# Kernel tuning notes

Hardware: AMD Instinct MI355X
Metric: run time of the kernel (lower is better)

Reference implementation:

```python
import jax, jax.numpy as jnp
import numpy as np

N, E, G = 20000, 320000, 8
H, C = 4, 64
NODE_IN, EDGE_IN, HID = 18, 4, 64
NEG = 0.2    # GATv2 leaky_relu negative slope
EPS = 1e-5   # BatchNorm eps (eval mode: running_mean=0, running_var=1)


def setup_inputs() -> dict:
    key = jax.random.key(0)
    ks = iter(jax.random.split(key, 48))
    rn = lambda shape, s=0.05: jax.random.normal(next(ks), shape, dtype=jnp.float32) * s
    return {
        "x": jax.random.normal(next(ks), (N, NODE_IN), dtype=jnp.float32),
        "edge_attr": jax.random.uniform(next(ks), (E, EDGE_IN), dtype=jnp.float32),
        "enc_w1": rn((NODE_IN, HID)), "enc_b1": jnp.zeros((HID,), jnp.float32),
        "enc_w2": rn((HID, HID)), "enc_b2": jnp.zeros((HID,), jnp.float32),
        "g1_wl": rn((HID, H * C)), "g1_wr": rn((HID, H * C)), "g1_we": rn((EDGE_IN, H * C)),
        "g1_att": rn((H, C)), "g1_b": jnp.zeros((H * C,), jnp.float32),
        "bn1_g": jnp.ones((H * C,), jnp.float32), "bn1_b": jnp.zeros((H * C,), jnp.float32),
        "g2_wl": rn((H * C, H * C)), "g2_wr": rn((H * C, H * C)), "g2_we": rn((EDGE_IN, H * C)),
        "g2_att": rn((H, C)), "g2_b": jnp.zeros((C,), jnp.float32),
        "bn2_g": jnp.ones((C,), jnp.float32), "bn2_b": jnp.zeros((C,), jnp.float32),
        "sage_wl": rn((HID, HID)), "sage_bl": jnp.zeros((HID,), jnp.float32), "sage_wr": rn((HID, HID)),
        "bn3_g": jnp.ones((HID,), jnp.float32), "bn3_b": jnp.zeros((HID,), jnp.float32),
        "gh_w1": rn((2 * HID, HID)), "gh_b1": jnp.zeros((HID,), jnp.float32),
        "gh_w2": rn((HID, 32)), "gh_b2": jnp.zeros((32,), jnp.float32),
        "gh_w3": rn((32, 1)), "gh_b3": jnp.zeros((1,), jnp.float32),
        "eh_w1": rn((2 * HID + EDGE_IN, 32)), "eh_b1": jnp.zeros((32,), jnp.float32),
        "eh_w2": rn((32, 1)), "eh_b2": jnp.zeros((1,), jnp.float32),
        "edge_index": jax.random.randint(next(ks), (2, E), 0, N, dtype=jnp.int32),
        "batch": jnp.sort(jax.random.randint(next(ks), (N,), 0, G, dtype=jnp.int32)),
    }


def _segment_softmax(logits, seg, num):
    mx = jax.ops.segment_max(logits, seg, num_segments=num)
    ex = jnp.exp(logits - mx[seg])
    den = jax.ops.segment_sum(ex, seg, num_segments=num)
    return ex / den[seg]


def _gatv2(h, src, dst, ea, wl, wr, we, att, bias, concat):
    n = h.shape[0]
    xl = (h @ wl).reshape(n, H, C)   # messages come from x_l[src]
    xr = (h @ wr).reshape(n, H, C)
    ee = (ea @ we).reshape(-1, H, C)
    m = xl[src] + xr[dst] + ee                                    # [E', H, C]
    logit = jnp.einsum('ehc,hc->eh', jax.nn.leaky_relu(m, NEG), att)
    alpha = _segment_softmax(logit, dst, n)                       # [E', H]
    out = jax.ops.segment_sum(alpha[:, :, None] * xl[src], dst, num_segments=n)
    if concat:
        return out.reshape(n, H * C) + bias
    return out.mean(axis=1) + bias


def _bn_eval(h, g, b):
    # eval-mode BatchNorm with running_mean=0, running_var=1
    return h * (g / jnp.sqrt(1.0 + EPS)) + b


def reference(x, edge_attr, enc_w1, enc_b1, enc_w2, enc_b2,
              g1_wl, g1_wr, g1_we, g1_att, g1_b, bn1_g, bn1_b,
              g2_wl, g2_wr, g2_we, g2_att, g2_b, bn2_g, bn2_b,
              sage_wl, sage_bl, sage_wr, bn3_g, bn3_b,
              gh_w1, gh_b1, gh_w2, gh_b2, gh_w3, gh_b3,
              eh_w1, eh_b1, eh_w2, eh_b2, edge_index, batch):
    src, dst = edge_index[0], edge_index[1]
    # PyG add_self_loops with fill_value='mean': loop edge_attr = mean of incoming edge_attr
    ones = jnp.ones((E,), jnp.float32)
    cnt = jax.ops.segment_sum(ones, dst, num_segments=N)
    loop_attr = jax.ops.segment_sum(edge_attr, dst, num_segments=N) / jnp.clip(cnt, 1.0)[:, None]
    sl = jnp.arange(N, dtype=src.dtype)
    src_sl = jnp.concatenate([src, sl])
    dst_sl = jnp.concatenate([dst, sl])
    ea_sl = jnp.concatenate([edge_attr, loop_attr], axis=0)

    # ZoneEncoder (dropout inactive in eval)
    h = jax.nn.relu(x @ enc_w1 + enc_b1) @ enc_w2 + enc_b2
    h = _gatv2(h, src_sl, dst_sl, ea_sl, g1_wl, g1_wr, g1_we, g1_att, g1_b, True)
    h = jax.nn.elu(_bn_eval(h, bn1_g, bn1_b))
    h = _gatv2(h, src_sl, dst_sl, ea_sl, g2_wl, g2_wr, g2_we, g2_att, g2_b, False)
    h = jax.nn.elu(_bn_eval(h, bn2_g, bn2_b))
    # SAGEConv: lin_l(mean_{j->i} h_j) + lin_r(h_i), no self loops
    agg = jax.ops.segment_sum(h[src], dst, num_segments=N) / jnp.clip(cnt, 1.0)[:, None]
    h = agg @ sage_wl + sage_bl + h @ sage_wr
    h = jax.nn.relu(_bn_eval(h, bn3_g, bn3_b))
    # global mean + max pooling per graph
    cntg = jax.ops.segment_sum(jnp.ones((N,), jnp.float32), batch, num_segments=G)
    mean_p = jax.ops.segment_sum(h, batch, num_segments=G) / jnp.clip(cntg, 1.0)[:, None]
    max_p = jax.ops.segment_max(h, batch, num_segments=G)
    hp = jnp.concatenate([mean_p, max_p], axis=-1)                # [G, 128]
    z = jax.nn.relu(hp @ gh_w1 + gh_b1)
    z = jax.nn.relu(z @ gh_w2 + gh_b2)
    graph_score = jax.nn.sigmoid(z @ gh_w3 + gh_b3)               # [G, 1]
    ef = jnp.concatenate([h[src], h[dst], edge_attr], axis=-1)    # [E, 132]
    ez = jax.nn.relu(ef @ eh_w1 + eh_b1)
    edge_scores = jax.nn.sigmoid(ez @ eh_w2 + eh_b2)              # [E, 1]
    return (graph_score, edge_scores)
```

## Files before the change

kernel.cpp:

```cpp
#include <hip/hip_runtime.h>

#define NN 20000
#define NE 320000
#define EP (NE + NN)
#define NG 8
#define HC 256
#define NODE_IN 18
#define HID 64
#define NEG_SLOPE 0.2f
#define BN_EPS 1e-5f

#define OFF_XL    0u
#define OFF_XR    5120000u
#define OFF_H1    10240000u
#define OFF_WTL   12800000u
#define OFF_WTR   12832768u
#define OFF_H3B   12865536u
#define OFF_WT1   13185536u
#define OFF_H0    15360000u
#define OFF_H3    16640000u
#define OFF_ZERO  18000000u
#define OFF_CNT   18000000u
#define OFF_PSUM  18020000u
#define OFF_PMAX  18020512u
#define OFF_PCNT  18021024u
#define ZERO_FLOATS (18021040u - 18000000u)
#define OFF_EACSR 18021040u
#define OFF_RP    19381040u
#define OFF_SRC   19421041u
#define OFF_BSUM  19761056u

#define SCAN_ELEM 1024
#define SCAN_NB ((NN + SCAN_ELEM - 1) / SCAN_ELEM)

typedef __attribute__((ext_vector_type(8))) short bf16x8_t;
typedef __attribute__((ext_vector_type(4))) float f32x4_t;

__device__ __forceinline__ ushort f2bf(float f) {
  unsigned u = __float_as_uint(f);
  unsigned r = (u + 0x7fffu + ((u >> 16) & 1u)) >> 16;
  return (ushort)r;
}
__device__ __forceinline__ float bf2f(ushort b) {
  return __uint_as_float(((unsigned)b) << 16);
}

__global__ __launch_bounds__(256) void k_count(
    const int* __restrict__ ei, unsigned* __restrict__ cnt, int* __restrict__ rank) {
  int e = blockIdx.x * 256 + threadIdx.x;
  if (e >= NE) return;
  int d = ei[NE + e];
  rank[e] = (int)atomicAdd(&cnt[d], 1u);
}

__global__ __launch_bounds__(256) void k_cast_wt(
    const float* __restrict__ Wl, const float* __restrict__ Wr,
    ushort* __restrict__ WtL, ushort* __restrict__ WtR) {
  int b = blockIdx.x;
  const float* W = (b < 256) ? Wl : Wr;
  ushort* Wt = (b < 256) ? WtL : WtR;
  int k = b & 255;
  int n = threadIdx.x;
  Wt[n * 256 + k] = f2bf(W[k * 256 + n]);
}

__global__ __launch_bounds__(256) void k_cast_eh(
    const float* __restrict__ w1, ushort* __restrict__ wt1) {
  int idx = blockIdx.x * 256 + threadIdx.x;
  int n = idx / 192, k = idx - n * 192;
  wt1[idx] = (k < 132) ? f2bf(w1[k * 32 + n]) : (ushort)0;
}

#define ENC_NPW 4
__global__ __launch_bounds__(256) void k_encoder(
    const float* __restrict__ x, const float* __restrict__ w1, const float* __restrict__ b1,
    const float* __restrict__ w2, const float* __restrict__ b2, float* __restrict__ h0) {
  __shared__ float W1[NODE_IN * HID];
  __shared__ float W2[HID * HID];
  __shared__ float B1s[HID];
  __shared__ float B2s[HID];
  __shared__ float hid_s[4][HID];
  const int tid = threadIdx.x;
  for (int i = tid; i < NODE_IN * HID; i += 256) W1[i] = w1[i];
  for (int i = tid; i < HID * HID; i += 256) W2[i] = w2[i];
  if (tid < HID) { B1s[tid] = b1[tid]; B2s[tid] = b2[tid]; }
  __syncthreads();
  const int lane = tid & 63;
  const int w = tid >> 6;
  #pragma unroll
  for (int t = 0; t < ENC_NPW; t++) {
    const int n = blockIdx.x * (4 * ENC_NPW) + w * ENC_NPW + t;
    const float* xp = &x[(size_t)n * NODE_IN];
    float s = B1s[lane];
    #pragma unroll
    for (int i = 0; i < NODE_IN; i++) s += xp[i] * W1[i * HID + lane];
    hid_s[w][lane] = fmaxf(s, 0.f);
    float o = B2s[lane];
    #pragma unroll 8
    for (int k = 0; k < HID; k++) o += hid_s[w][k] * W2[k * HID + lane];
    h0[(size_t)n * HID + lane] = o;
  }
}

__global__ __launch_bounds__(256) void k_scan_blk(
    const unsigned* __restrict__ cnt, int* __restrict__ row_ptr, int* __restrict__ bsums) {
  __shared__ int wsum[4];
  const int tid = threadIdx.x, lane = tid & 63, w = tid >> 6;
  const int i0 = blockIdx.x * SCAN_ELEM + tid * 4;
  int v0 = (i0 + 0 < NN) ? ((int)cnt[i0 + 0] + 1) : 0;
  int v1 = (i0 + 1 < NN) ? ((int)cnt[i0 + 1] + 1) : 0;
  int v2 = (i0 + 2 < NN) ? ((int)cnt[i0 + 2] + 1) : 0;
  int v3 = (i0 + 3 < NN) ? ((int)cnt[i0 + 3] + 1) : 0;
  int tsum = v0 + v1 + v2 + v3;
  int incl = tsum;
  #pragma unroll
  for (int off = 1; off < 64; off <<= 1) {
    int t = __shfl_up(incl, off);
    if (lane >= off) incl += t;
  }
  if (lane == 63) wsum[w] = incl;
  __syncthreads();
  int p = incl - tsum;
  #pragma unroll
  for (int k = 0; k < 4; k++) if (k < w) p += wsum[k];
  if (i0 + 0 < NN) row_ptr[i0 + 0] = p;
  if (i0 + 1 < NN) row_ptr[i0 + 1] = p + v0;
  if (i0 + 2 < NN) row_ptr[i0 + 2] = p + v0 + v1;
  if (i0 + 3 < NN) row_ptr[i0 + 3] = p + v0 + v1 + v2;
  if (tid == 0) bsums[blockIdx.x] = wsum[0] + wsum[1] + wsum[2] + wsum[3];
}

__global__ __launch_bounds__(256) void k_scan_add(
    const int* __restrict__ bsums, int* __restrict__ row_ptr) {
  const int b = blockIdx.x, tid = threadIdx.x;
  int off = 0;
  for (int j = 0; j < b; j++) off += bsums[j];
  const int i0 = b * SCAN_ELEM + tid * 4;
  #pragma unroll
  for (int k = 0; k < 4; k++) {
    int i = i0 + k;
    if (i < NN) row_ptr[i] += off;
  }
  if (b == 0 && tid == 0) row_ptr[NN] = EP;
}

__global__ __launch_bounds__(256) void k_csr_scatter(
    const int* __restrict__ ei, const int* __restrict__ rank,
    const int* __restrict__ row_ptr, const float* __restrict__ ea,
    int* __restrict__ srcs, float* __restrict__ ea_csr) {
  int e = blockIdx.x * 256 + threadIdx.x;
  if (e >= NE) return;
  int s = ei[e], d = ei[NE + e];
  int p = row_ptr[d] + rank[e];
  srcs[p] = s;
  *(float4*)&ea_csr[(size_t)p * 4] = *(const float4*)&ea[(size_t)e * 4];
}

__global__ __launch_bounds__(256) void k_loop_row(
    const int* __restrict__ row_ptr, int* __restrict__ srcs, float* __restrict__ ea_csr) {
  int i = blockIdx.x * 256 + threadIdx.x;
  if (i >= NN) return;
  int start = row_ptr[i], last = row_ptr[i + 1] - 1;
  float sx = 0.f, sy = 0.f, sz = 0.f, sw = 0.f;
  for (int j = start; j < last; ++j) {
    float4 a = *(const float4*)&ea_csr[(size_t)j * 4];
    sx += a.x; sy += a.y; sz += a.z; sw += a.w;
  }
  float c = (float)(last - start);
  if (c < 1.f) c = 1.f;
  float rc = 1.f / c;
  float4 o = {sx * rc, sy * rc, sz * rc, sw * rc};
  *(float4*)&ea_csr[(size_t)last * 4] = o;
  srcs[last] = i | (int)0x80000000;
}

template <int K, int OBF>
__global__ __launch_bounds__(256) void k_gemm256(
    const float* __restrict__ A, const float* __restrict__ W, void* __restrict__ OUTv) {
  __shared__ float Wl[32 * 256];
  __shared__ float Al[32 * 36];
  const int tid = threadIdx.x;
  const int n0 = blockIdx.x * 32;
  const int tx = tid & 63, ty = tid >> 6;
  float acc[8][4];
  #pragma unroll
  for (int m = 0; m < 8; m++)
    #pragma unroll
    for (int c = 0; c < 4; c++) acc[m][c] = 0.f;

  for (int kt = 0; kt < K; kt += 32) {
    #pragma unroll
    for (int r = 0; r < 8; r++) {
      int i4 = tid + 256 * r;
      int row = i4 >> 6;
      int col4 = (i4 & 63) * 4;
      *(float4*)&Wl[row * 256 + col4] = *(const float4*)&W[(size_t)(kt + row) * 256 + col4];
    }
    {
      int m = tid >> 3, kk = (tid & 7) * 4;
      float4 av = *(const float4*)&A[(size_t)(n0 + m) * K + kt + kk];
      Al[(kk + 0) * 36 + m] = av.x;
      Al[(kk + 1) * 36 + m] = av.y;
      Al[(kk + 2) * 36 + m] = av.z;
      Al[(kk + 3) * 36 + m] = av.w;
    }
    __syncthreads();
    #pragma unroll 8
    for (int k = 0; k < 32; k++) {
      float4 b = *(float4*)&Wl[k * 256 + tx * 4];
      float4 a0v = *(float4*)&Al[k * 36 + ty * 8];
      float4 a1v = *(float4*)&Al[k * 36 + ty * 8 + 4];
      float am[8] = {a0v.x, a0v.y, a0v.z, a0v.w, a1v.x, a1v.y, a1v.z, a1v.w};
      #pragma unroll
      for (int m = 0; m < 8; m++) {
        acc[m][0] += am[m] * b.x;
        acc[m][1] += am[m] * b.y;
        acc[m][2] += am[m] * b.z;
        acc[m][3] += am[m] * b.w;
      }
    }
    __syncthreads();
  }
  if (OBF) {
    ushort* OUT = (ushort*)OUTv;
    #pragma unroll
    for (int m = 0; m < 8; m++) {
      ushort4 o = {f2bf(acc[m][0]), f2bf(acc[m][1]), f2bf(acc[m][2]), f2bf(acc[m][3])};
      *(ushort4*)&OUT[(size_t)(n0 + ty * 8 + m) * 256 + tx * 4] = o;
    }
  } else {
    float* OUT = (float*)OUTv;
    #pragma unroll
    for (int m = 0; m < 8; m++) {
      float4 o = {acc[m][0], acc[m][1], acc[m][2], acc[m][3]};
      *(float4*)&OUT[(size_t)(n0 + ty * 8 + m) * 256 + tx * 4] = o;
    }
  }
}

template <int OBF>
__global__ __launch_bounds__(256) void k_gemm_mfma(
    const ushort* __restrict__ A, const ushort* __restrict__ Wt, void* __restrict__ OUTv) {
  __shared__ ushort Asub[32][72];
  __shared__ ushort Wsub[256][72];
  const int tid = threadIdx.x;
  const int lane = tid & 63;
  const int w = tid >> 6;
  const int n0 = blockIdx.x * 32;
  const int lr = lane & 15;
  const int lk = (lane >> 4) * 8;

  f32x4_t acc[2][4];
  #pragma unroll
  for (int m = 0; m < 2; m++)
    #pragma unroll
    for (int n = 0; n < 4; n++) acc[m][n] = (f32x4_t){0.f, 0.f, 0.f, 0.f};

  for (int kt = 0; kt < 256; kt += 64) {
    {
      int r = tid >> 3, seg = (tid & 7) * 8;
      *(uint4*)&Asub[r][seg] = *(const uint4*)&A[(size_t)(n0 + r) * 256 + kt + seg];
    }
    #pragma unroll
    for (int rep = 0; rep < 8; rep++) {
      int idx = rep * 256 + tid;
      int r = idx >> 3, seg = (idx & 7) * 8;
      *(uint4*)&Wsub[r][seg] = *(const uint4*)&Wt[(size_t)r * 256 + kt + seg];
    }
    __syncthreads();
    #pragma unroll
    for (int kk = 0; kk < 2; kk++) {
      bf16x8_t af0 = *(bf16x8_t*)&Asub[lr][kk * 32 + lk];
      bf16x8_t af1 = *(bf16x8_t*)&Asub[16 + lr][kk * 32 + lk];
      #pragma unroll
      for (int n = 0; n < 4; n++) {
        bf16x8_t bfr = *(bf16x8_t*)&Wsub[w * 64 + n * 16 + lr][kk * 32 + lk];
        acc[0][n] = __builtin_amdgcn_mfma_f32_16x16x32_bf16(af0, bfr, acc[0][n], 0, 0, 0);
        acc[1][n] = __builtin_amdgcn_mfma_f32_16x16x32_bf16(af1, bfr, acc[1][n], 0, 0, 0);
      }
    }
    __syncthreads();
  }
  const int crow = (lane >> 4) * 4;
  #pragma unroll
  for (int m = 0; m < 2; m++) {
    #pragma unroll
    for (int n = 0; n < 4; n++) {
      int col = w * 64 + n * 16 + lr;
      #pragma unroll
      for (int r = 0; r < 4; r++) {
        int row = n0 + m * 16 + crow + r;
        if (OBF) ((ushort*)OUTv)[(size_t)row * 256 + col] = f2bf(acc[m][n][r]);
        else     ((float*)OUTv)[(size_t)row * 256 + col] = acc[m][n][r];
      }
    }
  }
}

#define GAT_EDGE(A_, U_, DN_, C0_, C1_, C2_, C3_)                                  \
  {                                                                                \
    float xx_ = bf2f((U_).x), xy_ = bf2f((U_).y), xz_ = bf2f((U_).z), xw_ = bf2f((U_).w); \
    float m0_ = xx_ + xrd.x + (A_).x * we0.x + (A_).y * we1.x + (A_).z * we2.x + (A_).w * we3.x; \
    float m1_ = xy_ + xrd.y + (A_).x * we0.y + (A_).y * we1.y + (A_).z * we2.y + (A_).w * we3.y; \
    float m2_ = xz_ + xrd.z + (A_).x * we0.z + (A_).y * we1.z + (A_).z * we2.z + (A_).w * we3.z; \
    float m3_ = xw_ + xrd.w + (A_).x * we0.w + (A_).y * we1.w + (A_).z * we2.w + (A_).w * we3.w; \
    m0_ = fmaxf(m0_, NEG_SLOPE * m0_);                                             \
    m1_ = fmaxf(m1_, NEG_SLOPE * m1_);                                             \
    m2_ = fmaxf(m2_, NEG_SLOPE * m2_);                                             \
    m3_ = fmaxf(m3_, NEG_SLOPE * m3_);                                             \
    float lg_ = m0_ * attv.x + m1_ * attv.y + m2_ * attv.z + m3_ * attv.w;         \
    lg_ += __shfl_xor(lg_, 1);                                                     \
    lg_ += __shfl_xor(lg_, 2);                                                     \
    lg_ += __shfl_xor(lg_, 4);                                                     \
    lg_ += __shfl_xor(lg_, 8);                                                     \
    float p_ = __expf(lg_);                                                        \
    DN_ += p_;                                                                     \
    C0_ = fmaf(p_, xx_, C0_);                                                      \
    C1_ = fmaf(p_, xy_, C1_);                                                      \
    C2_ = fmaf(p_, xz_, C2_);                                                      \
    C3_ = fmaf(p_, xw_, C3_);                                                      \
  }

template <int CONCAT>
__global__ __launch_bounds__(256) void k_gat_fused(
    const ushort* __restrict__ xl, const float* __restrict__ xr,
    const float* __restrict__ we, const float* __restrict__ att,
    const int* __restrict__ srcs, const float* __restrict__ ea_csr,
    const int* __restrict__ row_ptr,
    const float* __restrict__ bias, const float* __restrict__ bng,
    const float* __restrict__ bnb, void* __restrict__ outp) {
  const int lane = threadIdx.x & 63;
  const int w = threadIdx.x >> 6;
  const int i = blockIdx.x * 4 + w;
  const int c0 = lane * 4;

  const float4 attv = *(const float4*)&att[c0];
  const float4 we0 = *(const float4*)&we[0 * HC + c0];
  const float4 we1 = *(const float4*)&we[1 * HC + c0];
  const float4 we2 = *(const float4*)&we[2 * HC + c0];
  const float4 we3 = *(const float4*)&we[3 * HC + c0];
  const float4 xrd = *(const float4*)&xr[(size_t)i * HC + c0];

  const int start = row_ptr[i];
  const int deg = row_ptr[i + 1] - start;

  float dnA = 0.f, aA0 = 0.f, aA1 = 0.f, aA2 = 0.f, aA3 = 0.f;
  float dnB = 0.f, aB0 = 0.f, aB1 = 0.f, aB2 = 0.f, aB3 = 0.f;

  for (int base = 0; base < deg; base += 64) {
    int rem = deg - base;
    if (rem > 64) rem = 64;
    int sv = 0;
    if (lane < rem) sv = srcs[start + base + lane] & 0x7fffffff;
    int jj = 0;
    for (; jj + 2 <= rem; jj += 2) {
      int s0 = __shfl(sv, jj);
      int s1 = __shfl(sv, jj + 1);
      float4 a0 = *(const float4*)&ea_csr[(size_t)(start + base + jj) * 4];
      float4 a1 = *(const float4*)&ea_csr[(size_t)(start + base + jj + 1) * 4];
      ushort4 u0 = *(const ushort4*)&xl[(size_t)s0 * HC + c0];
      ushort4 u1 = *(const ushort4*)&xl[(size_t)s1 * HC + c0];
      GAT_EDGE(a0, u0, dnA, aA0, aA1, aA2, aA3);
      GAT_EDGE(a1, u1, dnB, aB0, aB1, aB2, aB3);
    }
    if (jj < rem) {
      int s0 = __shfl(sv, jj);
      float4 a0 = *(const float4*)&ea_csr[(size_t)(start + base + jj) * 4];
      ushort4 u0 = *(const ushort4*)&xl[(size_t)s0 * HC + c0];
      GAT_EDGE(a0, u0, dnA, aA0, aA1, aA2, aA3);
    }
  }

  float rinv = 1.f / (dnA + dnB);
  float acc0 = (aA0 + aB0) * rinv;
  float acc1 = (aA1 + aB1) * rinv;
  float acc2 = (aA2 + aB2) * rinv;
  float acc3 = (aA3 + aB3) * rinv;

  const float inv_sqrt = rsqrtf(1.f + BN_EPS);
  if (CONCAT) {
    float4 bi = *(const float4*)&bias[c0];
    float4 g = *(const float4*)&bng[c0];
    float4 bb = *(const float4*)&bnb[c0];
    float v0 = (acc0 + bi.x) * (g.x * inv_sqrt) + bb.x;
    float v1 = (acc1 + bi.y) * (g.y * inv_sqrt) + bb.y;
    float v2 = (acc2 + bi.z) * (g.z * inv_sqrt) + bb.z;
    float v3 = (acc3 + bi.w) * (g.w * inv_sqrt) + bb.w;
    v0 = (v0 > 0.f) ? v0 : (__expf(v0) - 1.f);
    v1 = (v1 > 0.f) ? v1 : (__expf(v1) - 1.f);
    v2 = (v2 > 0.f) ? v2 : (__expf(v2) - 1.f);
    v3 = (v3 > 0.f) ? v3 : (__expf(v3) - 1.f);
    ushort* op = (ushort*)outp;
    ushort4 o = {f2bf(v0), f2bf(v1), f2bf(v2), f2bf(v3)};
    *(ushort4*)&op[(size_t)i * HC + c0] = o;
  } else {
    acc0 += __shfl_xor(acc0, 16); acc0 += __shfl_xor(acc0, 32);
    acc1 += __shfl_xor(acc1, 16); acc1 += __shfl_xor(acc1, 32);
    acc2 += __shfl_xor(acc2, 16); acc2 += __shfl_xor(acc2, 32);
    acc3 += __shfl_xor(acc3, 16); acc3 += __shfl_xor(acc3, 32);
    if (lane < 16) {
      int cc = lane * 4;
      float4 bi = *(const float4*)&bias[cc];
      float4 g = *(const float4*)&bng[cc];
      float4 bb = *(const float4*)&bnb[cc];
      float v0 = (0.25f * acc0 + bi.x) * (g.x * inv_sqrt) + bb.x;
      float v1 = (0.25f * acc1 + bi.y) * (g.y * inv_sqrt) + bb.y;
      float v2 = (0.25f * acc2 + bi.z) * (g.z * inv_sqrt) + bb.z;
      float v3 = (0.25f * acc3 + bi.w) * (g.w * inv_sqrt) + bb.w;
      v0 = (v0 > 0.f) ? v0 : (__expf(v0) - 1.f);
      v1 = (v1 > 0.f) ? v1 : (__expf(v1) - 1.f);
      v2 = (v2 > 0.f) ? v2 : (__expf(v2) - 1.f);
      v3 = (v3 > 0.f) ? v3 : (__expf(v3) - 1.f);
      float* op = (float*)outp;
      float4 o = {v0, v1, v2, v3};
      *(float4*)&op[(size_t)i * 64 + cc] = o;
    }
  }
}

__global__ __launch_bounds__(256) void k_sage(
    const float* __restrict__ h2, const int* __restrict__ row_ptr,
    const int* __restrict__ srcs, const unsigned* __restrict__ cnt,
    const float* __restrict__ wl, const float* __restrict__ bl,
    const float* __restrict__ wr, const float* __restrict__ bng,
    const float* __restrict__ bnb, float* __restrict__ h3,
    ushort* __restrict__ h3b) {
  __shared__ float agg_s[4][64];
  __shared__ float h2_s[4][64];
  int lane = threadIdx.x & 63;
  int w = threadIdx.x >> 6;
  int i = blockIdx.x * 4 + w;
  int start = row_ptr[i];
  int nreal = row_ptr[i + 1] - 1 - start;
  float a0 = 0.f, a1 = 0.f, a2 = 0.f, a3 = 0.f;
  for (int base = 0; base < nreal; base += 64) {
    int rem = nreal - base;
    if (rem > 64) rem = 64;
    int sv = 0;
    if (lane < rem) sv = srcs[start + base + lane];
    int jj = 0;
    for (; jj + 4 <= rem; jj += 4) {
      int s0 = __shfl(sv, jj);
      int s1 = __shfl(sv, jj + 1);
      int s2 = __shfl(sv, jj + 2);
      int s3 = __shfl(sv, jj + 3);
      a0 += h2[(size_t)s0 * 64 + lane];
      a1 += h2[(size_t)s1 * 64 + lane];
      a2 += h2[(size_t)s2 * 64 + lane];
      a3 += h2[(size_t)s3 * 64 + lane];
    }
    for (; jj < rem; ++jj) {
      int s0 = __shfl(sv, jj);
      a0 += h2[(size_t)s0 * 64 + lane];
    }
  }
  float a = (a0 + a1) + (a2 + a3);
  float c = (float)cnt[i];
  if (c < 1.f) c = 1.f;
  agg_s[w][lane] = a / c;
  h2_s[w][lane] = h2[(size_t)i * 64 + lane];
  __syncthreads();
  float s = bl[lane];
  #pragma unroll 4
  for (int k = 0; k < 64; k++)
    s += agg_s[w][k] * wl[k * 64 + lane] + h2_s[w][k] * wr[k * 64 + lane];
  s = s * (bng[lane] * rsqrtf(1.f + BN_EPS)) + bnb[lane];
  s = fmaxf(s, 0.f);
  h3[(size_t)i * 64 + lane] = s;
  h3b[(size_t)i * 64 + lane] = f2bf(s);
}

__global__ __launch_bounds__(256) void k_pool(
    const float* __restrict__ h3, const int* __restrict__ batch,
    float* __restrict__ psum, float* __restrict__ pmax, float* __restrict__ pcnt) {
  int j = threadIdx.x & 63, grp = threadIdx.x >> 6;
  int nbase = blockIdx.x * 256 + grp * 64;
  float s = 0.f, m = 0.f, cn = 0.f;
  int cur = -1;
  for (int t = 0; t < 64; t++) {
    int n = nbase + t;
    if (n >= NN) break;
    int g = batch[n];
    if (g != cur) {
      if (cur >= 0) {
        atomicAdd(&psum[cur * 64 + j], s);
        atomicMax((int*)&pmax[cur * 64 + j], __float_as_int(m));
        if (j == 0) atomicAdd(&pcnt[cur], cn);
      }
      cur = g; s = 0.f; m = 0.f; cn = 0.f;
    }
    float v = h3[(size_t)n * 64 + j];
    s += v; m = fmaxf(m, v); cn += 1.f;
  }
  if (cur >= 0) {
    atomicAdd(&psum[cur * 64 + j], s);
    atomicMax((int*)&pmax[cur * 64 + j], __float_as_int(m));
    if (j == 0) atomicAdd(&pcnt[cur], cn);
  }
}

__global__ void k_graph_head(
    const float* __restrict__ psum, const float* __restrict__ pmax,
    const float* __restrict__ pcnt,
    const float* __restrict__ w1, const float* __restrict__ b1,
    const float* __restrict__ w2, const float* __restrict__ b2,
    const float* __restrict__ w3, const float* __restrict__ b3,
    float* __restrict__ out) {
  __shared__ float hp[128];
  __shared__ float z1[64];
  __shared__ float z2[32];
  int g = blockIdx.x, j = threadIdx.x;
  float c = pcnt[g];
  if (c < 1.f) c = 1.f;
  hp[j] = psum[g * 64 + j] / c;
  hp[64 + j] = pmax[g * 64 + j];
  __syncthreads();
  float s = b1[j];
  #pragma unroll 8
  for (int k = 0; k < 128; k++) s += hp[k] * w1[k * 64 + j];
  z1[j] = fmaxf(s, 0.f);
  __syncthreads();
  if (j < 32) {
    float s2 = b2[j];
    #pragma unroll 8
    for (int k = 0; k < 64; k++) s2 += z1[k] * w2[k * 32 + j];
    z2[j] = fmaxf(s2, 0.f);
  }
  __syncthreads();
  if (j == 0) {
    float s3 = b3[0];
    #pragma unroll
    for (int k = 0; k < 32; k++) s3 += z2[k] * w3[k];
    out[g] = 1.f / (1.f + expf(-s3));
  }
}

__global__ __launch_bounds__(256) void k_edge_head(
    const ushort* __restrict__ h3b, const int* __restrict__ ei,
    const float* __restrict__ ea, const ushort* __restrict__ wt1,
    const float* __restrict__ b1, const float* __restrict__ w2,
    const float* __restrict__ b2, float* __restrict__ out) {
  __shared__ ushort Asub[64][192];
  __shared__ ushort Wsub[32][192];
  const int tid = threadIdx.x;
  const int e0 = blockIdx.x * 64;
  for (int idx = tid; idx < 768; idx += 256)
    *(uint4*)&(&Wsub[0][0])[idx * 8] = *(const uint4*)&wt1[idx * 8];
  for (int idx = tid; idx < 768; idx += 256) {
    int r = idx / 12, g = idx - r * 12;
    int e = e0 + r;
    ushort tmp[16];
    if (g < 8) {
      int node = (g < 4) ? ei[e] : ei[NE + e];
      int gc = (g & 3) * 16;
      *(uint4*)&tmp[0] = *(const uint4*)&h3b[(size_t)node * 64 + gc];
      *(uint4*)&tmp[8] = *(const uint4*)&h3b[(size_t)node * 64 + gc + 8];
    } else if (g == 8) {
      float4 a = *(const float4*)&ea[(size_t)e * 4];
      tmp[0] = f2bf(a.x); tmp[1] = f2bf(a.y); tmp[2] = f2bf(a.z); tmp[3] = f2bf(a.w);
      #pragma unroll
      for (int j = 4; j < 16; j++) tmp[j] = 0;
    } else {
      #pragma unroll
      for (int j = 0; j < 16; j++) tmp[j] = 0;
    }
    *(uint4*)&Asub[r][g * 16] = *(uint4*)&tmp[0];
    *(uint4*)&Asub[r][g * 16 + 8] = *(uint4*)&tmp[8];
  }
  __syncthreads();
  const int lane = tid & 63, wid = tid >> 6;
  const int lr = lane & 15, lk = (lane >> 4) * 8;
  f32x4_t acc0 = (f32x4_t){0.f, 0.f, 0.f, 0.f};
  f32x4_t acc1 = (f32x4_t){0.f, 0.f, 0.f, 0.f};
  #pragma unroll
  for (int ks = 0; ks < 6; ks++) {
    bf16x8_t af = *(bf16x8_t*)&Asub[wid * 16 + lr][ks * 32 + lk];
    bf16x8_t bw0 = *(bf16x8_t*)&Wsub[lr][ks * 32 + lk];
    bf16x8_t bw1 = *(bf16x8_t*)&Wsub[16 + lr][ks * 32 + lk];
    acc0 = __builtin_amdgcn_mfma_f32_16x16x32_bf16(af, bw0, acc0, 0, 0, 0);
    acc1 = __builtin_amdgcn_mfma_f32_16x16x32_bf16(af, bw1, acc1, 0, 0, 0);
  }
  float b1c0 = b1[lr], b1c1 = b1[16 + lr];
  float w2c0 = w2[lr], w2c1 = w2[16 + lr];
  float part[4];
  #pragma unroll
  for (int r = 0; r < 4; r++) {
    float v0 = fmaxf(acc0[r] + b1c0, 0.f) * w2c0;
    float v1 = fmaxf(acc1[r] + b1c1, 0.f) * w2c1;
    float p = v0 + v1;
    p += __shfl_xor(p, 1);
    p += __shfl_xor(p, 2);
    p += __shfl_xor(p, 4);
    p += __shfl_xor(p, 8);
    part[r] = p;
  }
  if (lr == 0) {
    const float bb2 = b2[0];
    int ebase = e0 + wid * 16 + (lane >> 4) * 4;
    #pragma unroll
    for (int r = 0; r < 4; r++)
      out[ebase + r] = 1.f / (1.f + __expf(-(part[r] + bb2)));
  }
}

extern "C" void kernel_launch(void* const* d_in, const int* in_sizes, int n_in,
                              void* d_out, int out_size, void* d_ws, size_t ws_size,
                              hipStream_t stream) {
  const float* x         = (const float*)d_in[0];
  const float* edge_attr = (const float*)d_in[1];
  const float* enc_w1 = (const float*)d_in[2];
  const float* enc_b1 = (const float*)d_in[3];
  const float* enc_w2 = (const float*)d_in[4];
  const float* enc_b2 = (const float*)d_in[5];
  const float* g1_wl = (const float*)d_in[6];
  const float* g1_wr = (const float*)d_in[7];
  const float* g1_we = (const float*)d_in[8];
  const float* g1_att = (const float*)d_in[9];
  const float* g1_b = (const float*)d_in[10];
  const float* bn1_g = (const float*)d_in[11];
  const float* bn1_b = (const float*)d_in[12];
  const float* g2_wl = (const float*)d_in[13];
  const float* g2_wr = (const float*)d_in[14];
  const float* g2_we = (const float*)d_in[15];
  const float* g2_att = (const float*)d_in[16];
  const float* g2_b = (const float*)d_in[17];
  const float* bn2_g = (const float*)d_in[18];
  const float* bn2_b = (const float*)d_in[19];
  const float* sage_wl = (const float*)d_in[20];
  const float* sage_bl = (const float*)d_in[21];
  const float* sage_wr = (const float*)d_in[22];
  const float* bn3_g = (const float*)d_in[23];
  const float* bn3_b = (const float*)d_in[24];
  const float* gh_w1 = (const float*)d_in[25];
  const float* gh_b1 = (const float*)d_in[26];
  const float* gh_w2 = (const float*)d_in[27];
  const float* gh_b2 = (const float*)d_in[28];
  const float* gh_w3 = (const float*)d_in[29];
  const float* gh_b3 = (const float*)d_in[30];
  const float* eh_w1 = (const float*)d_in[31];
  const float* eh_b1 = (const float*)d_in[32];
  const float* eh_w2 = (const float*)d_in[33];
  const float* eh_b2 = (const float*)d_in[34];
  const int* ei    = (const int*)d_in[35];
  const int* batch = (const int*)d_in[36];
  float* out = (float*)d_out;

  float* ws = (float*)d_ws;
  ushort* xlbf = (ushort*)(ws + OFF_XL);
  float* xr = ws + OFF_XR;
  ushort* h1bf = (ushort*)(ws + OFF_H1);
  ushort* wtl = (ushort*)(ws + OFF_WTL);
  ushort* wtr = (ushort*)(ws + OFF_WTR);
  ushort* h3b = (ushort*)(ws + OFF_H3B);
  ushort* wt1e = (ushort*)(ws + OFF_WT1);
  float* h0 = ws + OFF_H0;
  float* h3 = ws + OFF_H3;
  unsigned* cnt = (unsigned*)(ws + OFF_CNT);
  float* psum = ws + OFF_PSUM;
  float* pmax = ws + OFF_PMAX;
  float* pcnt = ws + OFF_PCNT;
  float* ea_csr = ws + OFF_EACSR;
  int* row_ptr = (int*)(ws + OFF_RP);
  int* srcs = (int*)(ws + OFF_SRC);
  int* bsums = (int*)(ws + OFF_BSUM);
  int* rank = (int*)(ws + OFF_XL);

  hipMemsetAsync(ws + OFF_ZERO, 0, ZERO_FLOATS * sizeof(float), stream);

  k_count<<<NE / 256, 256, 0, stream>>>(ei, cnt, rank);
  k_cast_wt<<<512, 256, 0, stream>>>(g2_wl, g2_wr, wtl, wtr);
  k_cast_eh<<<24, 256, 0, stream>>>(eh_w1, wt1e);
  k_encoder<<<NN / (4 * ENC_NPW), 256, 0, stream>>>(x, enc_w1, enc_b1, enc_w2, enc_b2, h0);
  k_scan_blk<<<SCAN_NB, 256, 0, stream>>>(cnt, row_ptr, bsums);
  k_scan_add<<<SCAN_NB, 256, 0, stream>>>(bsums, row_ptr);
  k_csr_scatter<<<NE / 256, 256, 0, stream>>>(ei, rank, row_ptr, edge_attr, srcs, ea_csr);
  k_loop_row<<<(NN + 255) / 256, 256, 0, stream>>>(row_ptr, srcs, ea_csr);

  k_gemm256<64, 1><<<NN / 32, 256, 0, stream>>>(h0, g1_wl, (void*)xlbf);
  k_gemm256<64, 0><<<NN / 32, 256, 0, stream>>>(h0, g1_wr, (void*)xr);
  k_gat_fused<1><<<NN / 4, 256, 0, stream>>>(xlbf, xr, g1_we, g1_att, srcs, ea_csr,
                                             row_ptr, g1_b, bn1_g, bn1_b, (void*)h1bf);

  k_gemm_mfma<1><<<NN / 32, 256, 0, stream>>>(h1bf, wtl, (void*)xlbf);
  k_gemm_mfma<0><<<NN / 32, 256, 0, stream>>>(h1bf, wtr, (void*)xr);
  k_gat_fused<0><<<NN / 4, 256, 0, stream>>>(xlbf, xr, g2_we, g2_att, srcs, ea_csr,
                                             row_ptr, g2_b, bn2_g, bn2_b, (void*)h0);

  k_sage<<<NN / 4, 256, 0, stream>>>(h0, row_ptr, srcs, cnt, sage_wl, sage_bl, sage_wr,
                                     bn3_g, bn3_b, h3, h3b);

  k_pool<<<(NN + 255) / 256, 256, 0, stream>>>(h3, batch, psum, pmax, pcnt);
  k_graph_head<<<NG, 64, 0, stream>>>(psum, pmax, pcnt, gh_w1, gh_b1, gh_w2, gh_b2, gh_w3, gh_b3, out);
  k_edge_head<<<NE / 64, 256, 0, stream>>>(h3b, ei, edge_attr, wt1e, eh_b1, eh_w2, eh_b2, out + NG);
}
```

Before: 346.8 us.

## Merge paired GEMM and cast launches, parallelize loop-row mean, pad edge-head LDS

Merges the two weight-cast kernels into one launch, and merges each pair of left/right projection GEMMs (fp32 and MFMA) into a single launch that picks its weight and output by block index. The self-loop edge-attribute mean now uses one wavefront per node with a shuffle reduction instead of one thread per node. The edge-head shared-memory rows are padded from 192 to 200 elements to reduce LDS bank conflicts. The aim is lower launch overhead and better parallelism in small kernels. The cost is a per-block branch and some extra LDS.

```diff
diff --git a/kernel.cpp b/kernel.cpp
--- a/kernel.cpp
+++ b/kernel.cpp
@@ -32,6 +32,7 @@
 
 #define SCAN_ELEM 1024
 #define SCAN_NB ((NN + SCAN_ELEM - 1) / SCAN_ELEM)
+#define NB32 (NN / 32)
 
 typedef __attribute__((ext_vector_type(8))) short bf16x8_t;
 typedef __attribute__((ext_vector_type(4))) float f32x4_t;
@@ -53,22 +54,22 @@
   rank[e] = (int)atomicAdd(&cnt[d], 1u);
 }
 
-__global__ __launch_bounds__(256) void k_cast_wt(
+__global__ __launch_bounds__(256) void k_cast_all(
     const float* __restrict__ Wl, const float* __restrict__ Wr,
-    ushort* __restrict__ WtL, ushort* __restrict__ WtR) {
+    const float* __restrict__ w1eh,
+    ushort* __restrict__ WtL, ushort* __restrict__ WtR, ushort* __restrict__ wt1) {
   int b = blockIdx.x;
-  const float* W = (b < 256) ? Wl : Wr;
-  ushort* Wt = (b < 256) ? WtL : WtR;
-  int k = b & 255;
-  int n = threadIdx.x;
-  Wt[n * 256 + k] = f2bf(W[k * 256 + n]);
-}
-
-__global__ __launch_bounds__(256) void k_cast_eh(
-    const float* __restrict__ w1, ushort* __restrict__ wt1) {
-  int idx = blockIdx.x * 256 + threadIdx.x;
-  int n = idx / 192, k = idx - n * 192;
-  wt1[idx] = (k < 132) ? f2bf(w1[k * 32 + n]) : (ushort)0;
+  if (b < 512) {
+    const float* W = (b < 256) ? Wl : Wr;
+    ushort* Wt = (b < 256) ? WtL : WtR;
+    int k = b & 255;
+    int n = threadIdx.x;
+    Wt[n * 256 + k] = f2bf(W[k * 256 + n]);
+  } else {
+    int idx = (b - 512) * 256 + threadIdx.x;
+    int n = idx / 192, k = idx - n * 192;
+    wt1[idx] = (k < 132) ? f2bf(w1eh[k * 32 + n]) : (ushort)0;
+  }
 }
 
 #define ENC_NPW 4
@@ -158,29 +159,32 @@
 
 __global__ __launch_bounds__(256) void k_loop_row(
     const int* __restrict__ row_ptr, int* __restrict__ srcs, float* __restrict__ ea_csr) {
-  int i = blockIdx.x * 256 + threadIdx.x;
-  if (i >= NN) return;
+  int lane = threadIdx.x & 63, w = threadIdx.x >> 6;
+  int i = blockIdx.x * 4 + w;
   int start = row_ptr[i], last = row_ptr[i + 1] - 1;
-  float sx = 0.f, sy = 0.f, sz = 0.f, sw = 0.f;
-  for (int j = start; j < last; ++j) {
-    float4 a = *(const float4*)&ea_csr[(size_t)j * 4];
-    sx += a.x; sy += a.y; sz += a.z; sw += a.w;
-  }
+  float s = 0.f;
+  int base = start * 4;
+  int nfl = (last - start) * 4;
+  for (int f = lane; f < nfl; f += 64) s += ea_csr[base + f];
+  s += __shfl_xor(s, 4);
+  s += __shfl_xor(s, 8);
+  s += __shfl_xor(s, 16);
+  s += __shfl_xor(s, 32);
   float c = (float)(last - start);
   if (c < 1.f) c = 1.f;
-  float rc = 1.f / c;
-  float4 o = {sx * rc, sy * rc, sz * rc, sw * rc};
-  *(float4*)&ea_csr[(size_t)last * 4] = o;
-  srcs[last] = i | (int)0x80000000;
-}
-
-template <int K, int OBF>
-__global__ __launch_bounds__(256) void k_gemm256(
-    const float* __restrict__ A, const float* __restrict__ W, void* __restrict__ OUTv) {
-  __shared__ float Wl[32 * 256];
+  if (lane < 4) ea_csr[(size_t)last * 4 + lane] = s / c;
+  if (lane == 0) srcs[last] = i | (int)0x80000000;
+}
+
+__global__ __launch_bounds__(256) void k_gemm256_dual(
+    const float* __restrict__ A, const float* __restrict__ Wl_, const float* __restrict__ Wr_,
+    ushort* __restrict__ OUTbf, float* __restrict__ OUTf) {
+  const bool first = blockIdx.x < NB32;
+  const float* __restrict__ W = first ? Wl_ : Wr_;
+  const int n0 = (first ? blockIdx.x : blockIdx.x - NB32) * 32;
+  __shared__ float Wlds[32 * 256];
   __shared__ float Al[32 * 36];
   const int tid = threadIdx.x;
-  const int n0 = blockIdx.x * 32;
   const int tx = tid & 63, ty = tid >> 6;
   float acc[8][4];
   #pragma unroll
@@ -188,17 +192,17 @@
     #pragma unroll
     for (int c = 0; c < 4; c++) acc[m][c] = 0.f;
 
-  for (int kt = 0; kt < K; kt += 32) {
+  for (int kt = 0; kt < 64; kt += 32) {
     #pragma unroll
     for (int r = 0; r < 8; r++) {
       int i4 = tid + 256 * r;
       int row = i4 >> 6;
       int col4 = (i4 & 63) * 4;
-      *(float4*)&Wl[row * 256 + col4] = *(const float4*)&W[(size_t)(kt + row) * 256 + col4];
+      *(float4*)&Wlds[row * 256 + col4] = *(const float4*)&W[(size_t)(kt + row) * 256 + col4];
     }
     {
       int m = tid >> 3, kk = (tid & 7) * 4;
-      float4 av = *(const float4*)&A[(size_t)(n0 + m) * K + kt + kk];
+      float4 av = *(const float4*)&A[(size_t)(n0 + m) * 64 + kt + kk];
       Al[(kk + 0) * 36 + m] = av.x;
       Al[(kk + 1) * 36 + m] = av.y;
       Al[(kk + 2) * 36 + m] = av.z;
@@ -207,7 +211,7 @@
     __syncthreads();
     #pragma unroll 8
     for (int k = 0; k < 32; k++) {
-      float4 b = *(float4*)&Wl[k * 256 + tx * 4];
+      float4 b = *(float4*)&Wlds[k * 256 + tx * 4];
       float4 a0v = *(float4*)&Al[k * 36 + ty * 8];
       float4 a1v = *(float4*)&Al[k * 36 + ty * 8 + 4];
       float am[8] = {a0v.x, a0v.y, a0v.z, a0v.w, a1v.x, a1v.y, a1v.z, a1v.w};
@@ -221,32 +225,32 @@
     }
     __syncthreads();
   }
-  if (OBF) {
-    ushort* OUT = (ushort*)OUTv;
+  if (first) {
     #pragma unroll
     for (int m = 0; m < 8; m++) {
       ushort4 o = {f2bf(acc[m][0]), f2bf(acc[m][1]), f2bf(acc[m][2]), f2bf(acc[m][3])};
-      *(ushort4*)&OUT[(size_t)(n0 + ty * 8 + m) * 256 + tx * 4] = o;
+      *(ushort4*)&OUTbf[(size_t)(n0 + ty * 8 + m) * 256 + tx * 4] = o;
     }
   } else {
-    float* OUT = (float*)OUTv;
     #pragma unroll
     for (int m = 0; m < 8; m++) {
       float4 o = {acc[m][0], acc[m][1], acc[m][2], acc[m][3]};
-      *(float4*)&OUT[(size_t)(n0 + ty * 8 + m) * 256 + tx * 4] = o;
-    }
-  }
-}
-
-template <int OBF>
-__global__ __launch_bounds__(256) void k_gemm_mfma(
-    const ushort* __restrict__ A, const ushort* __restrict__ Wt, void* __restrict__ OUTv) {
+      *(float4*)&OUTf[(size_t)(n0 + ty * 8 + m) * 256 + tx * 4] = o;
+    }
+  }
+}
+
+__global__ __launch_bounds__(256) void k_gemm_mfma_dual(
+    const ushort* __restrict__ A, const ushort* __restrict__ wtl,
+    const ushort* __restrict__ wtr, ushort* __restrict__ OUTbf, float* __restrict__ OUTf) {
+  const bool first = blockIdx.x < NB32;
+  const ushort* __restrict__ Wt = first ? wtl : wtr;
+  const int n0 = (first ? blockIdx.x : blockIdx.x - NB32) * 32;
   __shared__ ushort Asub[32][72];
   __shared__ ushort Wsub[256][72];
   const int tid = threadIdx.x;
   const int lane = tid & 63;
   const int w = tid >> 6;
-  const int n0 = blockIdx.x * 32;
   const int lr = lane & 15;
   const int lk = (lane >> 4) * 8;
 
@@ -290,8 +294,8 @@
       #pragma unroll
       for (int r = 0; r < 4; r++) {
         int row = n0 + m * 16 + crow + r;
-        if (OBF) ((ushort*)OUTv)[(size_t)row * 256 + col] = f2bf(acc[m][n][r]);
-        else     ((float*)OUTv)[(size_t)row * 256 + col] = acc[m][n][r];
+        if (first) OUTbf[(size_t)row * 256 + col] = f2bf(acc[m][n][r]);
+        else       OUTf[(size_t)row * 256 + col] = acc[m][n][r];
       }
     }
   }
@@ -540,12 +544,14 @@
     const float* __restrict__ ea, const ushort* __restrict__ wt1,
     const float* __restrict__ b1, const float* __restrict__ w2,
     const float* __restrict__ b2, float* __restrict__ out) {
-  __shared__ ushort Asub[64][192];
-  __shared__ ushort Wsub[32][192];
+  __shared__ ushort Asub[64][200];
+  __shared__ ushort Wsub[32][200];
   const int tid = threadIdx.x;
   const int e0 = blockIdx.x * 64;
-  for (int idx = tid; idx < 768; idx += 256)
-    *(uint4*)&(&Wsub[0][0])[idx * 8] = *(const uint4*)&wt1[idx * 8];
+  for (int idx = tid; idx < 768; idx += 256) {
+    int r = idx / 24, g8 = idx - r * 24;
+    *(uint4*)&Wsub[r][g8 * 8] = *(const uint4*)&wt1[(size_t)r * 192 + g8 * 8];
+  }
   for (int idx = tid; idx < 768; idx += 256) {
     int r = idx / 12, g = idx - r * 12;
     int e = e0 + r;
@@ -668,21 +674,18 @@
   hipMemsetAsync(ws + OFF_ZERO, 0, ZERO_FLOATS * sizeof(float), stream);
 
   k_count<<<NE / 256, 256, 0, stream>>>(ei, cnt, rank);
-  k_cast_wt<<<512, 256, 0, stream>>>(g2_wl, g2_wr, wtl, wtr);
-  k_cast_eh<<<24, 256, 0, stream>>>(eh_w1, wt1e);
+  k_cast_all<<<536, 256, 0, stream>>>(g2_wl, g2_wr, eh_w1, wtl, wtr, wt1e);
   k_encoder<<<NN / (4 * ENC_NPW), 256, 0, stream>>>(x, enc_w1, enc_b1, enc_w2, enc_b2, h0);
   k_scan_blk<<<SCAN_NB, 256, 0, stream>>>(cnt, row_ptr, bsums);
   k_scan_add<<<SCAN_NB, 256, 0, stream>>>(bsums, row_ptr);
   k_csr_scatter<<<NE / 256, 256, 0, stream>>>(ei, rank, row_ptr, edge_attr, srcs, ea_csr);
-  k_loop_row<<<(NN + 255) / 256, 256, 0, stream>>>(row_ptr, srcs, ea_csr);
-
-  k_gemm256<64, 1><<<NN / 32, 256, 0, stream>>>(h0, g1_wl, (void*)xlbf);
-  k_gemm256<64, 0><<<NN / 32, 256, 0, stream>>>(h0, g1_wr, (void*)xr);
+  k_loop_row<<<NN / 4, 256, 0, stream>>>(row_ptr, srcs, ea_csr);
+
+  k_gemm256_dual<<<2 * NB32, 256, 0, stream>>>(h0, g1_wl, g1_wr, xlbf, xr);
   k_gat_fused<1><<<NN / 4, 256, 0, stream>>>(xlbf, xr, g1_we, g1_att, srcs, ea_csr,
                                              row_ptr, g1_b, bn1_g, bn1_b, (void*)h1bf);
 
-  k_gemm_mfma<1><<<NN / 32, 256, 0, stream>>>(h1bf, wtl, (void*)xlbf);
-  k_gemm_mfma<0><<<NN / 32, 256, 0, stream>>>(h1bf, wtr, (void*)xr);
+  k_gemm_mfma_dual<<<2 * NB32, 256, 0, stream>>>(h1bf, wtl, wtr, xlbf, xr);
   k_gat_fused<0><<<NN / 4, 256, 0, stream>>>(xlbf, xr, g2_we, g2_att, srcs, ea_csr,
                                              row_ptr, g2_b, bn2_g, bn2_b, (void*)h0);
 
```

Result: faster. 323.3 us (-6.8%).
